# Optimization experiments

Hardware: AMD Instinct MI355X
Metric: run time of the kernel (lower is better)

Reference implementation:

```python
import jax, jax.numpy as jnp
import numpy as np

NUM_HEADS = 4
NUM_GROUPS = 8
EPS = 1e-5


def setup_inputs() -> dict:
    key = jax.random.key(0)
    ks = jax.random.split(key, 7)
    c = 256
    return {
        "x": jax.random.normal(ks[0], (4, c, 64, 64), jnp.float32),
        "gn_w": jax.random.normal(ks[1], (c,), jnp.float32),
        "gn_b": jax.random.normal(ks[2], (c,), jnp.float32),
        "qkv_w": jax.random.normal(ks[3], (3 * c, c), jnp.float32) * (c ** -0.5),
        "qkv_b": jax.random.normal(ks[4], (3 * c,), jnp.float32) * 0.02,
        "proj_w": jax.random.normal(ks[5], (c, c), jnp.float32) * (c ** -0.5),
        "proj_b": jax.random.normal(ks[6], (c,), jnp.float32) * 0.02,
    }


def reference(x, gn_w, gn_b, qkv_w, qkv_b, proj_w, proj_b):
    b, c, h, w = x.shape
    n = h * w
    hd = c // NUM_HEADS

    # GroupNorm(8, c)
    xg = x.reshape(b, NUM_GROUPS, -1)
    mu = jnp.mean(xg, axis=-1, keepdims=True)
    var = jnp.var(xg, axis=-1, keepdims=True)
    xn = ((xg - mu) * jax.lax.rsqrt(var + EPS)).reshape(b, c, h, w)
    xn = xn * gn_w[:, None, None] + gn_b[:, None, None]

    # 1x1 conv == channel matmul
    qkv = jnp.einsum('oc,bchw->bohw', qkv_w, xn) + qkv_b[:, None, None]
    q, k, v = jnp.split(qkv, 3, axis=1)
    q = q.reshape(b, NUM_HEADS, hd, n)
    k = k.reshape(b, NUM_HEADS, hd, n)
    v = v.reshape(b, NUM_HEADS, hd, n)

    scale = hd ** (-0.5)
    attn = jax.nn.softmax(jnp.einsum('bhcn,bhcm->bhnm', q * scale, k), axis=-1)
    out = jnp.einsum('bhnm,bhcm->bhcn', attn, v).reshape(b, c, h, w)

    return x + jnp.einsum('oc,bchw->bohw', proj_w, out) + proj_b[:, None, None]
```

## Files before the change

### kernel.cpp

```cpp
#include <hip/hip_runtime.h>
#include <hip/hip_bf16.h>

typedef unsigned short u16;
typedef __attribute__((ext_vector_type(4))) float f32x4;
typedef __attribute__((ext_vector_type(16))) float f32x16;
typedef __attribute__((ext_vector_type(8))) __bf16 bf16x8;
typedef __attribute__((ext_vector_type(2))) unsigned u32x2;

#define DEVI static __device__ __forceinline__
#define MFMA32 __builtin_amdgcn_mfma_f32_32x32x16_bf16

#if defined(__has_builtin)
#if __has_builtin(__builtin_amdgcn_exp2f)
#define HAVE_EXP2 1
#endif
#endif

#ifdef HAVE_EXP2
#define EXPX(x) __builtin_amdgcn_exp2f(x)
#define QSCALE 0.18033688011112042f
#define THRX 11.5f
#else
#define EXPX(x) __expf(x)
#define QSCALE 0.125f
#define THRX 8.0f
#endif

DEVI u16 f2bf(float f) {
    union { float f; unsigned u; } v; v.f = f;
    unsigned r = v.u + 0x7fffu + ((v.u >> 16) & 1u);
    return (u16)(r >> 16);
}

DEVI unsigned cvtpk(float lo, float hi_) {
    unsigned r;
    asm("v_cvt_pk_bf16_f32 %0, %1, %2" : "=v"(r) : "v"(lo), "v"(hi_));
    return r;
}

DEVI void plswap(unsigned a, unsigned b, unsigned& o0, unsigned& o1) {
#if defined(__has_builtin) && __has_builtin(__builtin_amdgcn_permlane32_swap)
    u32x2 r = __builtin_amdgcn_permlane32_swap(a, b, false, false);
    o0 = r[0]; o1 = r[1];
#else
    unsigned xa = (unsigned)__shfl_xor((int)a, 32, 64);
    unsigned xb = (unsigned)__shfl_xor((int)b, 32, 64);
    bool hi = (threadIdx.x & 32) != 0;
    o0 = hi ? xb : a;
    o1 = hi ? b : xa;
#endif
}

__global__ void __launch_bounds__(256) gn_stats_k(const float* __restrict__ x,
                                                  float* __restrict__ stats) {
    int bg = blockIdx.x;
    const float4* p = reinterpret_cast<const float4*>(x + (size_t)bg * 131072);
    float s = 0.f, s2 = 0.f;
    for (int i = threadIdx.x; i < 32768; i += 256) {
        float4 v = p[i];
        s  += v.x + v.y + v.z + v.w;
        s2 += v.x * v.x + v.y * v.y + v.z * v.z + v.w * v.w;
    }
    for (int off = 32; off; off >>= 1) {
        s  += __shfl_down(s,  off, 64);
        s2 += __shfl_down(s2, off, 64);
    }
    __shared__ float sb[8];
    int w = threadIdx.x >> 6, l = threadIdx.x & 63;
    if (l == 0) { sb[w] = s; sb[4 + w] = s2; }
    __syncthreads();
    if (threadIdx.x == 0) {
        float ts  = sb[0] + sb[1] + sb[2] + sb[3];
        float ts2 = sb[4] + sb[5] + sb[6] + sb[7];
        float mu  = ts * (1.f / 131072.f);
        float var = ts2 * (1.f / 131072.f) - mu * mu;
        stats[bg * 2]     = mu;
        stats[bg * 2 + 1] = rsqrtf(var + 1e-5f);
    }
}

__global__ void __launch_bounds__(256) convw_k(const float* __restrict__ qw,
                                               const float* __restrict__ pw,
                                               u16* __restrict__ wq,
                                               u16* __restrict__ wp) {
    int i = blockIdx.x * 256 + threadIdx.x;
    if (i < 196608) wq[i] = f2bf(qw[i]);
    if (i < 65536)  wp[i] = f2bf(pw[i]);
}

__global__ void __launch_bounds__(256) gnorm_t_k(const float* __restrict__ x,
                                                 const float* __restrict__ stats,
                                                 const float* __restrict__ gw,
                                                 const float* __restrict__ gb,
                                                 u16* __restrict__ xnT) {
    __shared__ float tile[32][33];
    int b = blockIdx.z, c0 = blockIdx.y * 32, n0 = blockIdx.x * 32;
    int tx = threadIdx.x, ty = threadIdx.y;
    const float* xb = x + ((size_t)b * 256 + c0) * 4096 + n0;
#pragma unroll
    for (int j = 0; j < 4; j++) {
        int r = ty + 8 * j;
        tile[r][tx] = xb[(size_t)r * 4096 + tx];
    }
    __syncthreads();
    int c = c0 + tx;
    int g = c >> 5;
    float mu = stats[(b * 8 + g) * 2], rs = stats[(b * 8 + g) * 2 + 1];
    float sc = rs * gw[c];
    float sh = gb[c] - mu * sc;
    u16* o = xnT + ((size_t)b * 4096 + n0) * 256 + c;
#pragma unroll
    for (int j = 0; j < 4; j++) {
        int r = ty + 8 * j;
        float v = tile[tx][r];
        o[(size_t)r * 256] = f2bf(v * sc + sh);
    }
}

__global__ void __launch_bounds__(256) qkv_gemm_k(const u16* __restrict__ wq,
                                                  const float* __restrict__ qkvb,
                                                  const u16* __restrict__ xnT,
                                                  u16* __restrict__ qT,
                                                  u16* __restrict__ kT,
                                                  u16* __restrict__ vv) {
    int b  = blockIdx.z;
    int w  = threadIdx.x >> 6, l = threadIdx.x & 63;
    int lr = l & 15, lg = l >> 4;
    int m0 = blockIdx.y * 64 + w * 16;
    int n0 = blockIdx.x * 64;
    f32x4 acc[4];
#pragma unroll
    for (int g = 0; g < 4; g++) acc[g] = (f32x4){0.f, 0.f, 0.f, 0.f};
    const u16* ap = wq + (size_t)(m0 + lr) * 256 + 8 * lg;
    const u16* bp = xnT + ((size_t)b * 4096 + n0 + lr) * 256 + 8 * lg;
#pragma unroll 2
    for (int k0 = 0; k0 < 256; k0 += 32) {
        bf16x8 a = *reinterpret_cast<const bf16x8*>(ap + k0);
#pragma unroll
        for (int g = 0; g < 4; g++) {
            bf16x8 bb = *reinterpret_cast<const bf16x8*>(bp + (size_t)g * 16 * 256 + k0);
            acc[g] = __builtin_amdgcn_mfma_f32_16x16x32_bf16(a, bb, acc[g], 0, 0, 0);
        }
    }
#pragma unroll
    for (int g = 0; g < 4; g++) {
#pragma unroll
        for (int j = 0; j < 4; j++) {
            int o = m0 + lg * 4 + j;
            int n = n0 + g * 16 + lr;
            float v = acc[g][j] + qkvb[o];
            int sec = o >> 8;
            int oc  = o & 255;
            int h = oc >> 6, ch = oc & 63;
            size_t bh = (size_t)(b * 4 + h);
            if (sec == 0)      qT[(bh * 4096 + n) * 64 + ch] = f2bf(v * QSCALE);
            else if (sec == 1) kT[(bh * 4096 + n) * 64 + ch] = f2bf(v);
            else               vv[(bh * 64 + ch) * 4096 + n] = f2bf(v);
        }
    }
}

__global__ void __launch_bounds__(256) attn_k(const u16* __restrict__ qT,
                                              const u16* __restrict__ kT,
                                              const u16* __restrict__ vv,
                                              u16* __restrict__ oT) {
    __shared__ __align__(16) u16 kbuf[2][2048];
    __shared__ __align__(16) u16 vbuf[2][2048];
    const int bh = blockIdx.y, b = bh >> 2, h = bh & 3;
    const int tid = threadIdx.x;
    const int w = tid >> 6, l = tid & 63;
    const int q5 = l & 31, hi = l >> 5;
    const int n0w = blockIdx.x * 128 + w * 32;
    const u16* qp = qT + (size_t)bh * 262144;
    const u16* kp = kT + (size_t)bh * 262144;
    const u16* vp = vv + (size_t)bh * 262144;

    const u16* qrow = qp + (size_t)(n0w + q5) * 64 + 8 * hi;
    const bf16x8 qf0 = *(const bf16x8*)(qrow);
    const bf16x8 qf1 = *(const bf16x8*)(qrow + 16);
    const bf16x8 qf2 = *(const bf16x8*)(qrow + 32);
    const bf16x8 qf3 = *(const bf16x8*)(qrow + 48);

    const int krow = 8 * w + (l >> 3);
    const int kw_lds = krow * 64 + (((l & 7) ^ (l >> 3)) << 3);
    const u16* kg = kp + (size_t)krow * 64 + (l & 7) * 8;
    const int vd = 16 * w + (l >> 2);
    const int vw_lds = vd * 32 + (((l & 3) ^ ((l >> 2) & 3)) << 3);
    const u16* vg = vp + (size_t)vd * 4096 + (l & 3) * 8;

    const int ksw = (q5 & 7) << 3;
    const int vsw = (q5 & 3) << 3;

    f32x16 o0, o1;
#pragma unroll
    for (int r = 0; r < 16; ++r) { o0[r] = 0.f; o1[r] = 0.f; }
    float mrun = -3.0e38f, lsum = 0.f;

    {
        bf16x8 k0 = *(const bf16x8*)(kg);
        bf16x8 v0 = *(const bf16x8*)(vg);
        *(bf16x8*)&kbuf[0][kw_lds] = k0;
        *(bf16x8*)&vbuf[0][vw_lds] = v0;
    }
    __syncthreads();

    int cur = 0;
    for (int it = 0; it < 128; ++it) {
        bf16x8 knx, vnx;
        const bool pre = (it < 127);
        if (pre) {
            knx = *(const bf16x8*)(kg + (size_t)(it + 1) * 2048);
            vnx = *(const bf16x8*)(vg + (it + 1) * 32);
        }
        f32x16 s;
#pragma unroll
        for (int r = 0; r < 16; ++r) s[r] = 0.f;
        {
            const u16* kb = &kbuf[cur][q5 * 64];
            s = MFMA32(*(const bf16x8*)(kb + ((8 * hi) ^ ksw)),      qf0, s, 0, 0, 0);
            s = MFMA32(*(const bf16x8*)(kb + ((16 + 8 * hi) ^ ksw)), qf1, s, 0, 0, 0);
            s = MFMA32(*(const bf16x8*)(kb + ((32 + 8 * hi) ^ ksw)), qf2, s, 0, 0, 0);
            s = MFMA32(*(const bf16x8*)(kb + ((48 + 8 * hi) ^ ksw)), qf3, s, 0, 0, 0);
        }
        float pm = s[0];
#pragma unroll
        for (int r = 1; r < 16; ++r) pm = fmaxf(pm, s[r]);
        pm = fmaxf(pm, __shfl_xor(pm, 32, 64));
        if (!__all(pm - mrun <= THRX)) {
            float mnew = fmaxf(mrun, pm);
            float al = EXPX(mrun - mnew);
            mrun = mnew;
            lsum *= al;
#pragma unroll
            for (int r = 0; r < 16; ++r) {
                float ar = __shfl(al, (r & 3) + 8 * (r >> 2) + 4 * hi, 64);
                o0[r] *= ar; o1[r] *= ar;
            }
        }
#pragma unroll
        for (int r = 0; r < 16; ++r) s[r] = EXPX(s[r] - mrun);
        float rs = 0.f;
#pragma unroll
        for (int r = 0; r < 16; ++r) rs += s[r];
        rs += __shfl_xor(rs, 32, 64);
        lsum += rs;
        unsigned c0 = cvtpk(s[0], s[1]),   c1 = cvtpk(s[2], s[3]);
        unsigned c2 = cvtpk(s[4], s[5]),   c3 = cvtpk(s[6], s[7]);
        unsigned c4 = cvtpk(s[8], s[9]),   c5 = cvtpk(s[10], s[11]);
        unsigned c6 = cvtpk(s[12], s[13]), c7 = cvtpk(s[14], s[15]);
        unsigned x0a, x0b, y0a, y0b, x1a, x1b, y1a, y1b;
        plswap(c0, c2, x0a, x0b);
        plswap(c1, c3, y0a, y0b);
        plswap(c4, c6, x1a, x1b);
        plswap(c5, c7, y1a, y1b);
        union { unsigned u[4]; bf16x8 v; } pa0, pa1;
        pa0.u[0] = x0a; pa0.u[1] = y0a; pa0.u[2] = x0b; pa0.u[3] = y0b;
        pa1.u[0] = x1a; pa1.u[1] = y1a; pa1.u[2] = x1b; pa1.u[3] = y1b;
        {
            const u16* vb0 = &vbuf[cur][(size_t)q5 * 32];
            const u16* vb1 = &vbuf[cur][(size_t)(32 + q5) * 32];
            bf16x8 v00 = *(const bf16x8*)(vb0 + ((8 * hi) ^ vsw));
            bf16x8 v10 = *(const bf16x8*)(vb0 + ((16 + 8 * hi) ^ vsw));
            bf16x8 v01 = *(const bf16x8*)(vb1 + ((8 * hi) ^ vsw));
            bf16x8 v11 = *(const bf16x8*)(vb1 + ((16 + 8 * hi) ^ vsw));
            o0 = MFMA32(pa0.v, v00, o0, 0, 0, 0);
            o0 = MFMA32(pa1.v, v10, o0, 0, 0, 0);
            o1 = MFMA32(pa0.v, v01, o1, 0, 0, 0);
            o1 = MFMA32(pa1.v, v11, o1, 0, 0, 0);
        }
        if (pre) {
            *(bf16x8*)&kbuf[cur ^ 1][kw_lds] = knx;
            *(bf16x8*)&vbuf[cur ^ 1][vw_lds] = vnx;
        }
        __syncthreads();
        cur ^= 1;
    }
    float linv = 1.f / lsum;
    u16* ob = oT + ((size_t)b * 4096 + n0w) * 256 + h * 64 + q5;
#pragma unroll
    for (int r = 0; r < 16; ++r) {
        int qo = (r & 3) + 8 * (r >> 2) + 4 * hi;
        float lr_ = __shfl(linv, qo, 64);
        ob[(size_t)qo * 256]      = f2bf(o0[r] * lr_);
        ob[(size_t)qo * 256 + 32] = f2bf(o1[r] * lr_);
    }
}

__global__ void __launch_bounds__(256) proj_gemm_k(const u16* __restrict__ wp,
                                                   const float* __restrict__ pb,
                                                   const u16* __restrict__ oT,
                                                   const float* __restrict__ x,
                                                   float* __restrict__ out) {
    int b  = blockIdx.z;
    int w  = threadIdx.x >> 6, l = threadIdx.x & 63;
    int lr = l & 15, lg = l >> 4;
    int m0 = blockIdx.y * 64 + w * 16;
    int n0 = blockIdx.x * 64;
    f32x4 acc[4];
#pragma unroll
    for (int g = 0; g < 4; g++) acc[g] = (f32x4){0.f, 0.f, 0.f, 0.f};
    const u16* ap = wp + (size_t)(m0 + lr) * 256 + 8 * lg;
    const u16* bp = oT + ((size_t)b * 4096 + n0 + lr) * 256 + 8 * lg;
#pragma unroll 2
    for (int k0 = 0; k0 < 256; k0 += 32) {
        bf16x8 a = *reinterpret_cast<const bf16x8*>(ap + k0);
#pragma unroll
        for (int g = 0; g < 4; g++) {
            bf16x8 bb = *reinterpret_cast<const bf16x8*>(bp + (size_t)g * 16 * 256 + k0);
            acc[g] = __builtin_amdgcn_mfma_f32_16x16x32_bf16(a, bb, acc[g], 0, 0, 0);
        }
    }
#pragma unroll
    for (int g = 0; g < 4; g++)
#pragma unroll
        for (int j = 0; j < 4; j++) {
            int o = m0 + lg * 4 + j;
            int n = n0 + g * 16 + lr;
            size_t idx = ((size_t)b * 256 + o) * 4096 + n;
            out[idx] = x[idx] + pb[o] + acc[g][j];
        }
}

extern "C" void kernel_launch(void* const* d_in, const int* in_sizes, int n_in,
                              void* d_out, int out_size, void* d_ws, size_t ws_size,
                              hipStream_t stream) {
    const float* x      = (const float*)d_in[0];
    const float* gn_w   = (const float*)d_in[1];
    const float* gn_b   = (const float*)d_in[2];
    const float* qkv_w  = (const float*)d_in[3];
    const float* qkv_b  = (const float*)d_in[4];
    const float* proj_w = (const float*)d_in[5];
    const float* proj_b = (const float*)d_in[6];
    float* out = (float*)d_out;

    char* ws = (char*)d_ws;
    float* stats = (float*)(ws + 0);
    u16* wq  = (u16*)(ws + 256);
    u16* wp  = (u16*)(ws + 393472);
    u16* xnT = (u16*)(ws + 524544);
    u16* qT  = (u16*)(ws + 8913152);
    u16* kT  = (u16*)(ws + 17301760);
    u16* vv  = (u16*)(ws + 25690368);
    u16* oT  = (u16*)(ws + 34078976);

    gn_stats_k<<<dim3(32), dim3(256), 0, stream>>>(x, stats);
    convw_k<<<dim3(768), dim3(256), 0, stream>>>(qkv_w, proj_w, wq, wp);
    gnorm_t_k<<<dim3(128, 8, 4), dim3(32, 8), 0, stream>>>(x, stats, gn_w, gn_b, xnT);
    qkv_gemm_k<<<dim3(64, 12, 4), dim3(256), 0, stream>>>(wq, qkv_b, xnT, qT, kT, vv);
    attn_k<<<dim3(32, 16), dim3(256), 0, stream>>>(qT, kT, vv, oT);
    proj_gemm_k<<<dim3(64, 4, 4), dim3(256), 0, stream>>>(wp, proj_b, oT, x, out);
}
```

Baseline: 315.5 us.

## Split GN stats, stage QKV epilogue in LDS, enlarge attention KV tiles with direct-to-LDS loads

GroupNorm statistics are now computed by 256 blocks writing partial sums, followed by a tiny reduction kernel, replacing 32 long-running blocks. The QKV GEMM epilogue stages results in shared memory so q/k/v are written with coalesced 16-byte stores instead of scattered 2-byte stores. The attention kernel processes 64 keys per iteration, loads K/V straight into LDS with global_load_lds and a new swizzle, and raises wave priority around MFMA blocks. These changes target underused parallelism, uncoalesced writes and per-iteration sync overhead, at the cost of more LDS use and an extra launch.

```diff
diff --git a/kernel.cpp b/kernel.cpp
--- a/kernel.cpp
+++ b/kernel.cpp
@@ -51,12 +51,19 @@
 #endif
 }
 
-__global__ void __launch_bounds__(256) gn_stats_k(const float* __restrict__ x,
-                                                  float* __restrict__ stats) {
-    int bg = blockIdx.x;
-    const float4* p = reinterpret_cast<const float4*>(x + (size_t)bg * 131072);
+DEVI void gld16(const u16* g, u16* l) {
+    __builtin_amdgcn_global_load_lds(
+        (const __attribute__((address_space(1))) unsigned int*)g,
+        (__attribute__((address_space(3))) unsigned int*)l, 16, 0, 0);
+}
+
+__global__ void __launch_bounds__(256) gn_stats1_k(const float* __restrict__ x,
+                                                   float* __restrict__ part) {
+    int bid = blockIdx.x;
+    int bg = bid >> 3, seg = bid & 7;
+    const float4* p = reinterpret_cast<const float4*>(x + (size_t)bg * 131072 + seg * 16384);
     float s = 0.f, s2 = 0.f;
-    for (int i = threadIdx.x; i < 32768; i += 256) {
+    for (int i = threadIdx.x; i < 4096; i += 256) {
         float4 v = p[i];
         s  += v.x + v.y + v.z + v.w;
         s2 += v.x * v.x + v.y * v.y + v.z * v.z + v.w * v.w;
@@ -70,12 +77,21 @@
     if (l == 0) { sb[w] = s; sb[4 + w] = s2; }
     __syncthreads();
     if (threadIdx.x == 0) {
-        float ts  = sb[0] + sb[1] + sb[2] + sb[3];
-        float ts2 = sb[4] + sb[5] + sb[6] + sb[7];
-        float mu  = ts * (1.f / 131072.f);
-        float var = ts2 * (1.f / 131072.f) - mu * mu;
-        stats[bg * 2]     = mu;
-        stats[bg * 2 + 1] = rsqrtf(var + 1e-5f);
+        part[bid * 2]     = sb[0] + sb[1] + sb[2] + sb[3];
+        part[bid * 2 + 1] = sb[4] + sb[5] + sb[6] + sb[7];
+    }
+}
+
+__global__ void gn_stats2_k(const float* __restrict__ part, float* __restrict__ stats) {
+    int t = threadIdx.x;
+    if (t < 32) {
+        float s = 0.f, s2 = 0.f;
+#pragma unroll
+        for (int i = 0; i < 8; i++) { s += part[(t * 8 + i) * 2]; s2 += part[(t * 8 + i) * 2 + 1]; }
+        float mu  = s * (1.f / 131072.f);
+        float var = s2 * (1.f / 131072.f) - mu * mu;
+        stats[t * 2]     = mu;
+        stats[t * 2 + 1] = rsqrtf(var + 1e-5f);
     }
 }
 
@@ -123,10 +139,12 @@
                                                   u16* __restrict__ qT,
                                                   u16* __restrict__ kT,
                                                   u16* __restrict__ vv) {
+    __shared__ __align__(16) u16 T[64 * 72];
     int b  = blockIdx.z;
     int w  = threadIdx.x >> 6, l = threadIdx.x & 63;
     int lr = l & 15, lg = l >> 4;
-    int m0 = blockIdx.y * 64 + w * 16;
+    int m0b = blockIdx.y * 64;
+    int m0 = m0b + w * 16;
     int n0 = blockIdx.x * 64;
     f32x4 acc[4];
 #pragma unroll
@@ -142,21 +160,39 @@
             acc[g] = __builtin_amdgcn_mfma_f32_16x16x32_bf16(a, bb, acc[g], 0, 0, 0);
         }
     }
+    int sec  = m0b >> 8;
+    int hsec = (m0b >> 6) & 3;
+    float qs = (sec == 0) ? QSCALE : 1.f;
 #pragma unroll
     for (int g = 0; g < 4; g++) {
+        ushort4 pk;
 #pragma unroll
         for (int j = 0; j < 4; j++) {
             int o = m0 + lg * 4 + j;
-            int n = n0 + g * 16 + lr;
-            float v = acc[g][j] + qkvb[o];
-            int sec = o >> 8;
-            int oc  = o & 255;
-            int h = oc >> 6, ch = oc & 63;
-            size_t bh = (size_t)(b * 4 + h);
-            if (sec == 0)      qT[(bh * 4096 + n) * 64 + ch] = f2bf(v * QSCALE);
-            else if (sec == 1) kT[(bh * 4096 + n) * 64 + ch] = f2bf(v);
-            else               vv[(bh * 64 + ch) * 4096 + n] = f2bf(v);
-        }
+            float v = (acc[g][j] + qkvb[o]) * qs;
+            ((u16*)&pk)[j] = f2bf(v);
+        }
+        if (sec < 2) {
+            *(ushort4*)&T[(g * 16 + lr) * 72 + w * 16 + lg * 4] = pk;
+        } else {
+#pragma unroll
+            for (int j = 0; j < 4; j++)
+                T[(w * 16 + lg * 4 + j) * 72 + g * 16 + lr] = ((u16*)&pk)[j];
+        }
+    }
+    __syncthreads();
+    int row = threadIdx.x >> 2;
+    u16* dst;
+    if (sec < 2) {
+        u16* base = (sec == 0 ? qT : kT);
+        dst = base + ((size_t)(b * 4 + hsec) * 4096 + n0 + row) * 64;
+    } else {
+        dst = vv + ((size_t)(b * 4 + hsec) * 64 + row) * 4096 + n0;
+    }
+#pragma unroll
+    for (int p = 0; p < 2; p++) {
+        int c = (threadIdx.x & 3) + 4 * p;
+        *(ulonglong2*)(dst + c * 8) = *(const ulonglong2*)&T[row * 72 + c * 8];
     }
 }
 
@@ -164,11 +200,10 @@
                                               const u16* __restrict__ kT,
                                               const u16* __restrict__ vv,
                                               u16* __restrict__ oT) {
-    __shared__ __align__(16) u16 kbuf[2][2048];
-    __shared__ __align__(16) u16 vbuf[2][2048];
+    __shared__ __align__(16) u16 kbuf[2][4096];
+    __shared__ __align__(16) u16 vbuf[2][4096];
     const int bh = blockIdx.y, b = bh >> 2, h = bh & 3;
-    const int tid = threadIdx.x;
-    const int w = tid >> 6, l = tid & 63;
+    const int tid = threadIdx.x, w = tid >> 6, l = tid & 63;
     const int q5 = l & 31, hi = l >> 5;
     const int n0w = blockIdx.x * 128 + w * 32;
     const u16* qp = qT + (size_t)bh * 262144;
@@ -176,55 +211,58 @@
     const u16* vp = vv + (size_t)bh * 262144;
 
     const u16* qrow = qp + (size_t)(n0w + q5) * 64 + 8 * hi;
-    const bf16x8 qf0 = *(const bf16x8*)(qrow);
-    const bf16x8 qf1 = *(const bf16x8*)(qrow + 16);
-    const bf16x8 qf2 = *(const bf16x8*)(qrow + 32);
-    const bf16x8 qf3 = *(const bf16x8*)(qrow + 48);
-
-    const int krow = 8 * w + (l >> 3);
-    const int kw_lds = krow * 64 + (((l & 7) ^ (l >> 3)) << 3);
-    const u16* kg = kp + (size_t)krow * 64 + (l & 7) * 8;
-    const int vd = 16 * w + (l >> 2);
-    const int vw_lds = vd * 32 + (((l & 3) ^ ((l >> 2) & 3)) << 3);
-    const u16* vg = vp + (size_t)vd * 4096 + (l & 3) * 8;
-
-    const int ksw = (q5 & 7) << 3;
-    const int vsw = (q5 & 3) << 3;
+    bf16x8 qf[4];
+    qf[0] = *(const bf16x8*)(qrow);
+    qf[1] = *(const bf16x8*)(qrow + 16);
+    qf[2] = *(const bf16x8*)(qrow + 32);
+    qf[3] = *(const bf16x8*)(qrow + 48);
+
+    const int pr = l >> 3, pc = l & 7;
+    const int gswz = ((pc ^ pr) << 3);
+    const u16* kgl = kp + (size_t)(16 * w + pr) * 64 + gswz;
+    const u16* vgl = vp + (size_t)(16 * w + pr) * 4096 + gswz;
+    const int lbase = 1024 * w;
+    const int ksw = q5 & 7;
 
     f32x16 o0, o1;
 #pragma unroll
     for (int r = 0; r < 16; ++r) { o0[r] = 0.f; o1[r] = 0.f; }
     float mrun = -3.0e38f, lsum = 0.f;
 
-    {
-        bf16x8 k0 = *(const bf16x8*)(kg);
-        bf16x8 v0 = *(const bf16x8*)(vg);
-        *(bf16x8*)&kbuf[0][kw_lds] = k0;
-        *(bf16x8*)&vbuf[0][vw_lds] = v0;
-    }
+#define STAGE(BUF, IT)                                                        \
+    {                                                                         \
+        const u16* kt_ = kgl + (size_t)(IT) * 4096;                           \
+        const u16* vt_ = vgl + (size_t)(IT) * 64;                             \
+        gld16(kt_,         &kbuf[BUF][lbase]);                                \
+        gld16(kt_ + 512,   &kbuf[BUF][lbase + 512]);                          \
+        gld16(vt_,         &vbuf[BUF][lbase]);                                \
+        gld16(vt_ + 32768, &vbuf[BUF][lbase + 512]);                          \
+    }
+
+    STAGE(0, 0);
     __syncthreads();
 
     int cur = 0;
-    for (int it = 0; it < 128; ++it) {
-        bf16x8 knx, vnx;
-        const bool pre = (it < 127);
-        if (pre) {
-            knx = *(const bf16x8*)(kg + (size_t)(it + 1) * 2048);
-            vnx = *(const bf16x8*)(vg + (it + 1) * 32);
-        }
-        f32x16 s;
-#pragma unroll
-        for (int r = 0; r < 16; ++r) s[r] = 0.f;
-        {
-            const u16* kb = &kbuf[cur][q5 * 64];
-            s = MFMA32(*(const bf16x8*)(kb + ((8 * hi) ^ ksw)),      qf0, s, 0, 0, 0);
-            s = MFMA32(*(const bf16x8*)(kb + ((16 + 8 * hi) ^ ksw)), qf1, s, 0, 0, 0);
-            s = MFMA32(*(const bf16x8*)(kb + ((32 + 8 * hi) ^ ksw)), qf2, s, 0, 0, 0);
-            s = MFMA32(*(const bf16x8*)(kb + ((48 + 8 * hi) ^ ksw)), qf3, s, 0, 0, 0);
-        }
-        float pm = s[0];
-#pragma unroll
-        for (int r = 1; r < 16; ++r) pm = fmaxf(pm, s[r]);
+    for (int it = 0; it < 64; ++it) {
+        if (it < 63) STAGE(cur ^ 1, it + 1);
+        const u16* kb = &kbuf[cur][q5 * 64];
+        const u16* vb = &vbuf[cur][q5 * 64];
+        f32x16 s0, s1;
+#pragma unroll
+        for (int r = 0; r < 16; ++r) { s0[r] = 0.f; s1[r] = 0.f; }
+        __builtin_amdgcn_s_setprio(1);
+#pragma unroll
+        for (int st = 0; st < 4; ++st) {
+            int ch = ((hi + 2 * st) ^ ksw) << 3;
+            s0 = MFMA32(*(const bf16x8*)(kb + ch),        qf[st], s0, 0, 0, 0);
+            s1 = MFMA32(*(const bf16x8*)(kb + 2048 + ch), qf[st], s1, 0, 0, 0);
+        }
+        __builtin_amdgcn_s_setprio(0);
+        float pm = s0[0];
+#pragma unroll
+        for (int r = 1; r < 16; ++r) pm = fmaxf(pm, s0[r]);
+#pragma unroll
+        for (int r = 0; r < 16; ++r) pm = fmaxf(pm, s1[r]);
         pm = fmaxf(pm, __shfl_xor(pm, 32, 64));
         if (!__all(pm - mrun <= THRX)) {
             float mnew = fmaxf(mrun, pm);
@@ -237,44 +275,52 @@
                 o0[r] *= ar; o1[r] *= ar;
             }
         }
-#pragma unroll
-        for (int r = 0; r < 16; ++r) s[r] = EXPX(s[r] - mrun);
         float rs = 0.f;
 #pragma unroll
-        for (int r = 0; r < 16; ++r) rs += s[r];
+        for (int r = 0; r < 16; ++r) { s0[r] = EXPX(s0[r] - mrun); rs += s0[r]; }
+#pragma unroll
+        for (int r = 0; r < 16; ++r) { s1[r] = EXPX(s1[r] - mrun); rs += s1[r]; }
         rs += __shfl_xor(rs, 32, 64);
         lsum += rs;
-        unsigned c0 = cvtpk(s[0], s[1]),   c1 = cvtpk(s[2], s[3]);
-        unsigned c2 = cvtpk(s[4], s[5]),   c3 = cvtpk(s[6], s[7]);
-        unsigned c4 = cvtpk(s[8], s[9]),   c5 = cvtpk(s[10], s[11]);
-        unsigned c6 = cvtpk(s[12], s[13]), c7 = cvtpk(s[14], s[15]);
+        unsigned c0 = cvtpk(s0[0], s0[1]),   c1 = cvtpk(s0[2], s0[3]);
+        unsigned c2 = cvtpk(s0[4], s0[5]),   c3 = cvtpk(s0[6], s0[7]);
+        unsigned c4 = cvtpk(s0[8], s0[9]),   c5 = cvtpk(s0[10], s0[11]);
+        unsigned c6 = cvtpk(s0[12], s0[13]), c7 = cvtpk(s0[14], s0[15]);
+        unsigned d0 = cvtpk(s1[0], s1[1]),   d1 = cvtpk(s1[2], s1[3]);
+        unsigned d2 = cvtpk(s1[4], s1[5]),   d3 = cvtpk(s1[6], s1[7]);
+        unsigned d4 = cvtpk(s1[8], s1[9]),   d5 = cvtpk(s1[10], s1[11]);
+        unsigned d6 = cvtpk(s1[12], s1[13]), d7 = cvtpk(s1[14], s1[15]);
         unsigned x0a, x0b, y0a, y0b, x1a, x1b, y1a, y1b;
-        plswap(c0, c2, x0a, x0b);
-        plswap(c1, c3, y0a, y0b);
-        plswap(c4, c6, x1a, x1b);
-        plswap(c5, c7, y1a, y1b);
-        union { unsigned u[4]; bf16x8 v; } pa0, pa1;
+        unsigned x2a, x2b, y2a, y2b, x3a, x3b, y3a, y3b;
+        plswap(c0, c2, x0a, x0b); plswap(c1, c3, y0a, y0b);
+        plswap(c4, c6, x1a, x1b); plswap(c5, c7, y1a, y1b);
+        plswap(d0, d2, x2a, x2b); plswap(d1, d3, y2a, y2b);
+        plswap(d4, d6, x3a, x3b); plswap(d5, d7, y3a, y3b);
+        union { unsigned u[4]; bf16x8 v; } pa0, pa1, pa2, pa3;
         pa0.u[0] = x0a; pa0.u[1] = y0a; pa0.u[2] = x0b; pa0.u[3] = y0b;
         pa1.u[0] = x1a; pa1.u[1] = y1a; pa1.u[2] = x1b; pa1.u[3] = y1b;
+        pa2.u[0] = x2a; pa2.u[1] = y2a; pa2.u[2] = x2b; pa2.u[3] = y2b;
+        pa3.u[0] = x3a; pa3.u[1] = y3a; pa3.u[2] = x3b; pa3.u[3] = y3b;
+        __builtin_amdgcn_s_setprio(1);
         {
-            const u16* vb0 = &vbuf[cur][(size_t)q5 * 32];
-            const u16* vb1 = &vbuf[cur][(size_t)(32 + q5) * 32];
-            bf16x8 v00 = *(const bf16x8*)(vb0 + ((8 * hi) ^ vsw));
-            bf16x8 v10 = *(const bf16x8*)(vb0 + ((16 + 8 * hi) ^ vsw));
-            bf16x8 v01 = *(const bf16x8*)(vb1 + ((8 * hi) ^ vsw));
-            bf16x8 v11 = *(const bf16x8*)(vb1 + ((16 + 8 * hi) ^ vsw));
-            o0 = MFMA32(pa0.v, v00, o0, 0, 0, 0);
-            o0 = MFMA32(pa1.v, v10, o0, 0, 0, 0);
-            o1 = MFMA32(pa0.v, v01, o1, 0, 0, 0);
-            o1 = MFMA32(pa1.v, v11, o1, 0, 0, 0);
-        }
-        if (pre) {
-            *(bf16x8*)&kbuf[cur ^ 1][kw_lds] = knx;
-            *(bf16x8*)&vbuf[cur ^ 1][vw_lds] = vnx;
-        }
+            int ch0 = ((0 + hi) ^ ksw) << 3;
+            int ch1 = ((2 + hi) ^ ksw) << 3;
+            int ch2 = ((4 + hi) ^ ksw) << 3;
+            int ch3 = ((6 + hi) ^ ksw) << 3;
+            o0 = MFMA32(pa0.v, *(const bf16x8*)(vb + ch0),        o0, 0, 0, 0);
+            o1 = MFMA32(pa0.v, *(const bf16x8*)(vb + 2048 + ch0), o1, 0, 0, 0);
+            o0 = MFMA32(pa1.v, *(const bf16x8*)(vb + ch1),        o0, 0, 0, 0);
+            o1 = MFMA32(pa1.v, *(const bf16x8*)(vb + 2048 + ch1), o1, 0, 0, 0);
+            o0 = MFMA32(pa2.v, *(const bf16x8*)(vb + ch2),        o0, 0, 0, 0);
+            o1 = MFMA32(pa2.v, *(const bf16x8*)(vb + 2048 + ch2), o1, 0, 0, 0);
+            o0 = MFMA32(pa3.v, *(const bf16x8*)(vb + ch3),        o0, 0, 0, 0);
+            o1 = MFMA32(pa3.v, *(const bf16x8*)(vb + 2048 + ch3), o1, 0, 0, 0);
+        }
+        __builtin_amdgcn_s_setprio(0);
         __syncthreads();
         cur ^= 1;
     }
+#undef STAGE
     float linv = 1.f / lsum;
     u16* ob = oT + ((size_t)b * 4096 + n0w) * 256 + h * 64 + q5;
 #pragma unroll
@@ -342,8 +388,10 @@
     u16* kT  = (u16*)(ws + 17301760);
     u16* vv  = (u16*)(ws + 25690368);
     u16* oT  = (u16*)(ws + 34078976);
-
-    gn_stats_k<<<dim3(32), dim3(256), 0, stream>>>(x, stats);
+    float* part = (float*)(ws + 42467584);
+
+    gn_stats1_k<<<dim3(256), dim3(256), 0, stream>>>(x, part);
+    gn_stats2_k<<<dim3(1), dim3(64), 0, stream>>>(part, stats);
     convw_k<<<dim3(768), dim3(256), 0, stream>>>(qkv_w, proj_w, wq, wp);
     gnorm_t_k<<<dim3(128, 8, 4), dim3(32, 8), 0, stream>>>(x, stats, gn_w, gn_b, xnT);
     qkv_gemm_k<<<dim3(64, 12, 4), dim3(256), 0, stream>>>(wq, qkv_b, xnT, qT, kT, vv);
```

After: 267.9 us. 1.18x faster.
